# Kernel optimization log

Hardware: AMD Instinct MI355X
Metric: run time of the kernel (lower is better)

Reference implementation:

```python
import jax, jax.numpy as jnp
import numpy as np

B, N, C, H = 8, 1024, 768, 12
D = C // H
SCALE = D ** -0.5


def _norm_unbiased(t):
    # per-head-dim standardization with torch's default unbiased std (ddof=1)
    mu = t.mean(axis=-1, keepdims=True)
    var = ((t - mu) ** 2).sum(axis=-1, keepdims=True) / (t.shape[-1] - 1)
    return (t - mu) / jnp.sqrt(var)


def setup_inputs() -> dict:
    key = jax.random.key(0)
    kx, kq, kp, kb = jax.random.split(key, 4)
    x = jax.random.normal(kx, (B, N, C), dtype=jnp.float32)
    # nn.Linear default init ~ U(-1/sqrt(fan_in), 1/sqrt(fan_in)); scale suffices
    s = 1.0 / np.sqrt(C)
    qkv_w = jax.random.uniform(kq, (3 * C, C), minval=-s, maxval=s, dtype=jnp.float32)
    proj_w = jax.random.uniform(kp, (C, C), minval=-s, maxval=s, dtype=jnp.float32)
    proj_b = jax.random.uniform(kb, (C,), minval=-s, maxval=s, dtype=jnp.float32)
    return {"x": x, "qkv_w": qkv_w, "proj_w": proj_w, "proj_b": proj_b}


def reference(x, qkv_w, proj_w, proj_b):
    Bn, Nn, Cn = x.shape
    qkv = x @ qkv_w.T                                   # [B,N,3C]
    qkv = qkv.reshape(Bn, Nn, 3, H, D).transpose(2, 0, 3, 1, 4)  # [3,B,H,N,D]
    q, k, v = qkv[0], qkv[1], qkv[2]
    q = _norm_unbiased(q)
    k = _norm_unbiased(k)
    attn = jax.nn.softmax(jnp.einsum('bhnd,bhmd->bhnm', q, k) * SCALE, axis=-1)
    out = jnp.einsum('bhnm,bhmd->bhnd', attn, v)        # [B,H,N,D]
    out = out.transpose(0, 2, 1, 3).reshape(Bn, Nn, Cn)  # [B,N,C]
    return out @ proj_w.T + proj_b
```

## Files before the change

kernel.cpp:

```cpp
#include <hip/hip_runtime.h>
#include <hip/hip_bf16.h>
#include <stdint.h>

typedef unsigned short u16;
typedef __attribute__((ext_vector_type(8))) short bf16x8;
typedef __attribute__((ext_vector_type(4))) float f32x4;

#define GLDS16(gsrc, ldst) \
  __builtin_amdgcn_global_load_lds((const __attribute__((address_space(1))) uint32_t*)(gsrc), \
                                   (__attribute__((address_space(3))) uint32_t*)(ldst), 16, 0, 0)

__device__ __forceinline__ u16 f2bf(float f) {
  unsigned u = __float_as_uint(f);
  unsigned r = (u + 0x7fffu + ((u >> 16) & 1u)) >> 16;
  return (u16)r;
}
__device__ __forceinline__ float bf2f(u16 v) {
  return __uint_as_float(((unsigned)v) << 16);
}

__global__ void cvt_f2b4(const float* __restrict__ in, u16* __restrict__ out, int n4) {
  int i = blockIdx.x * 256 + threadIdx.x;
  if (i < n4) {
    float4 v = ((const float4*)in)[i];
    ushort4 r;
    r.x = f2bf(v.x); r.y = f2bf(v.y); r.z = f2bf(v.z); r.w = f2bf(v.w);
    ((ushort4*)out)[i] = r;
  }
}

template<int OUT_BF16, int HAS_BIAS>
__global__ __launch_bounds__(256, 2)
void gemm_bt(const u16* __restrict__ A, const u16* __restrict__ Bm,
             const float* __restrict__ bias, void* __restrict__ Cout,
             int M, int N, int K)
{
  __shared__ __align__(16) u16 As[128 * 32];
  __shared__ __align__(16) u16 Bs[128 * 32];
  const int tid  = threadIdx.x;
  const int lane = tid & 63;
  const int w    = tid >> 6;
  const int wr   = w >> 1, wc = w & 1;
  const int m0 = blockIdx.x * 128;
  const int n0 = blockIdx.y * 128;

  f32x4 acc[4][4];
  for (int m = 0; m < 4; ++m)
    for (int n = 0; n < 4; ++n)
      acc[m][n] = (f32x4){0.f, 0.f, 0.f, 0.f};

  const int rsel = lane >> 2;
  const int koff = (lane & 3) * 8;
  const int fr   = lane & 15;
  const int fk   = (lane >> 4) * 8;

  const int KT = K >> 5;
  for (int kt = 0; kt < KT; ++kt) {
    const int kbase = kt * 32;
#pragma unroll
    for (int t = 0; t < 2; ++t) {
      const int seg = w * 2 + t;
      const int rr = seg * 16 + rsel;
      GLDS16(A  + (size_t)(m0 + rr) * K + kbase + koff, (char*)As + seg * 1024);
      GLDS16(Bm + (size_t)(n0 + rr) * K + kbase + koff, (char*)Bs + seg * 1024);
    }
    __syncthreads();
    bf16x8 af[4], bg[4];
#pragma unroll
    for (int m = 0; m < 4; ++m)
      af[m] = *(const bf16x8*)(As + (wr * 64 + m * 16 + fr) * 32 + fk);
#pragma unroll
    for (int n = 0; n < 4; ++n)
      bg[n] = *(const bf16x8*)(Bs + (wc * 64 + n * 16 + fr) * 32 + fk);
#pragma unroll
    for (int m = 0; m < 4; ++m)
#pragma unroll
      for (int n = 0; n < 4; ++n)
        acc[m][n] = __builtin_amdgcn_mfma_f32_16x16x32_bf16(af[m], bg[n], acc[m][n], 0, 0, 0);
    __syncthreads();
  }

  const int r0 = m0 + wr * 64 + (lane >> 4) * 4;
  const int c0 = n0 + wc * 64 + fr;
  float bv[4];
  if (HAS_BIAS) {
#pragma unroll
    for (int n = 0; n < 4; ++n) bv[n] = bias[c0 + n * 16];
  }
#pragma unroll
  for (int m = 0; m < 4; ++m)
#pragma unroll
    for (int n = 0; n < 4; ++n)
#pragma unroll
      for (int i = 0; i < 4; ++i) {
        const size_t idx = (size_t)(r0 + m * 16 + i) * N + (c0 + n * 16);
        if (OUT_BF16) ((u16*)Cout)[idx] = f2bf(acc[m][n][i]);
        else          ((float*)Cout)[idx] = acc[m][n][i] + (HAS_BIAS ? bv[n] : 0.f);
      }
}

__global__ void norm_qk(const u16* __restrict__ qkv, u16* __restrict__ q, u16* __restrict__ k) {
  const int lane = threadIdx.x & 63;
  const int w = threadIdx.x >> 6;
  const int r = blockIdx.x * 4 + w;
  const int b = r / 12288;
  const int rem = r - b * 12288;
  const int h = rem >> 10;
  const int n = rem & 1023;
  const size_t rowbase = (size_t)(b * 1024 + n) * 2304 + h * 64 + lane;
  const size_t obase = ((size_t)(b * 12 + h) * 1024 + n) * 64 + lane;
#pragma unroll
  for (int s = 0; s < 2; ++s) {
    float t = bf2f(qkv[rowbase + (size_t)s * 768]);
    float sum = t;
#pragma unroll
    for (int m = 1; m < 64; m <<= 1) sum += __shfl_xor(sum, m, 64);
    float mu = sum * (1.f / 64.f);
    float d = t - mu;
    float ss = d * d;
#pragma unroll
    for (int m = 1; m < 64; m <<= 1) ss += __shfl_xor(ss, m, 64);
    float outv = d * rsqrtf(ss * (1.f / 63.f));
    (s == 0 ? q : k)[obase] = f2bf(outv);
  }
}

__global__ void transpose_v(const u16* __restrict__ qkv, u16* __restrict__ vt) {
  __shared__ u16 tile[64][65];
  const int bid = blockIdx.x;
  const int nt = bid & 15;
  const int bh = bid >> 4;
  const int b = bh / 12, h = bh % 12;
  const int tx = threadIdx.x & 63;
  const int ty = threadIdx.x >> 6;
#pragma unroll
  for (int i = 0; i < 16; ++i) {
    const int n = i * 4 + ty;
    tile[n][tx] = qkv[(size_t)(b * 1024 + nt * 64 + n) * 2304 + 1536 + h * 64 + tx];
  }
  __syncthreads();
#pragma unroll
  for (int i = 0; i < 16; ++i) {
    const int d = i * 4 + ty;
    vt[((size_t)(bh * 64 + d)) * 1024 + nt * 64 + tx] = tile[tx][d];
  }
}

__global__ __launch_bounds__(256, 2)
void attn_fwd(const u16* __restrict__ q, const u16* __restrict__ k,
              const u16* __restrict__ vt, u16* __restrict__ out)
{
  __shared__ __align__(16) u16 Ks[2][64 * 64];
  __shared__ __align__(16) u16 VTs[2][64 * 64];
  __shared__ __align__(16) u16 Ps[4][16 * 64];
  const int tid = threadIdx.x, lane = tid & 63, w = tid >> 6;
  const int bid = (blockIdx.x & 7) * 192 + (blockIdx.x >> 3);
  const int qt = bid & 15;
  const int bh = bid >> 4;
  const int b = bh / 12, h = bh % 12;
  const int fr = lane & 15;
  const int hi = lane >> 4;
  const int fk = hi * 8;

  bf16x8 aq[2];
  {
    const int qrow = qt * 64 + w * 16 + fr;
    const u16* qp = q + ((size_t)bh * 1024 + qrow) * 64;
#pragma unroll
    for (int kk = 0; kk < 2; ++kk)
      aq[kk] = *(const bf16x8*)(qp + kk * 32 + fk);
  }

  f32x4 o[4];
  for (int n = 0; n < 4; ++n) o[n] = (f32x4){0.f, 0.f, 0.f, 0.f};
  float rs[4] = {0.f, 0.f, 0.f, 0.f};

  const int srow = lane >> 3;
  const int sc   = ((lane & 7) ^ srow) * 8;
  const u16* kg = k  + (size_t)bh * 65536;
  const u16* vg = vt + (size_t)bh * 65536;

  auto stage = [&](int buf, int kt) {
#pragma unroll
    for (int t = 0; t < 2; ++t) {
      const int seg = w * 2 + t;
      const int rr = seg * 8 + srow;
      GLDS16(kg + (size_t)(kt * 64 + rr) * 64 + sc,  (char*)Ks[buf]  + seg * 1024);
      GLDS16(vg + (size_t)rr * 1024 + kt * 64 + sc,  (char*)VTs[buf] + seg * 1024);
    }
  };

  int cur = 0;
  stage(0, 0);
  for (int kt = 0; kt < 16; ++kt) {
    __syncthreads();
    if (kt < 15) stage(cur ^ 1, kt + 1);

    f32x4 s[4];
#pragma unroll
    for (int n = 0; n < 4; ++n) s[n] = (f32x4){0.f, 0.f, 0.f, 0.f};
#pragma unroll
    for (int n = 0; n < 4; ++n)
#pragma unroll
      for (int kk = 0; kk < 2; ++kk) {
        bf16x8 bk = *(const bf16x8*)(Ks[cur] + (n * 16 + fr) * 64 + (((kk * 4 + hi) ^ (fr & 7)) * 8));
        s[n] = __builtin_amdgcn_mfma_f32_16x16x32_bf16(aq[kk], bk, s[n], 0, 0, 0);
      }

#pragma unroll
    for (int n = 0; n < 4; ++n)
#pragma unroll
      for (int i = 0; i < 4; ++i) {
        float p = __expf(s[n][i] * 0.125f);
        rs[i] += p;
        const int row = hi * 4 + i;
        const int swc = (n * 2 + (fr >> 3)) ^ (row & 7);
        Ps[w][row * 64 + swc * 8 + (fr & 7)] = f2bf(p);
      }

#pragma unroll
    for (int kk = 0; kk < 2; ++kk) {
      bf16x8 ap = *(const bf16x8*)(&Ps[w][fr * 64 + (((kk * 4 + hi) ^ (fr & 7)) * 8)]);
#pragma unroll
      for (int n = 0; n < 4; ++n) {
        bf16x8 bv = *(const bf16x8*)(VTs[cur] + (n * 16 + fr) * 64 + (((kk * 4 + hi) ^ (fr & 7)) * 8));
        o[n] = __builtin_amdgcn_mfma_f32_16x16x32_bf16(ap, bv, o[n], 0, 0, 0);
      }
    }
    cur ^= 1;
  }

  float inv[4];
#pragma unroll
  for (int i = 0; i < 4; ++i) {
    float v = rs[i];
    v += __shfl_xor(v, 1, 64);
    v += __shfl_xor(v, 2, 64);
    v += __shfl_xor(v, 4, 64);
    v += __shfl_xor(v, 8, 64);
    inv[i] = 1.f / v;
  }
  const int orow0 = qt * 64 + w * 16 + (lane >> 4) * 4;
#pragma unroll
  for (int n = 0; n < 4; ++n)
#pragma unroll
    for (int i = 0; i < 4; ++i)
      out[((size_t)b * 1024 + orow0 + i) * 768 + h * 64 + n * 16 + fr] = f2bf(o[n][i] * inv[i]);
}

extern "C" void kernel_launch(void* const* d_in, const int* in_sizes, int n_in,
                              void* d_out, int out_size, void* d_ws, size_t ws_size,
                              hipStream_t stream)
{
  (void)in_sizes; (void)n_in; (void)out_size; (void)ws_size;
  const float* x      = (const float*)d_in[0];
  const float* qkv_w  = (const float*)d_in[1];
  const float* proj_w = (const float*)d_in[2];
  const float* proj_b = (const float*)d_in[3];
  float* out = (float*)d_out;

  char* p = (char*)d_ws;
  auto take = [&](size_t bytes) { char* r = p; p += (bytes + 255) & ~(size_t)255; return r; };
  u16* xb   = (u16*)take((size_t)8192 * 768 * 2);
  u16* wqb  = (u16*)take((size_t)2304 * 768 * 2);
  u16* wpb  = (u16*)take((size_t)768 * 768 * 2);
  u16* qkvb = (u16*)take((size_t)8192 * 2304 * 2);
  u16* qb   = (u16*)take((size_t)8192 * 768 * 2);
  u16* kb   = (u16*)take((size_t)8192 * 768 * 2);
  u16* vtb  = (u16*)take((size_t)8192 * 768 * 2);
  u16* aob  = (u16*)take((size_t)8192 * 768 * 2);

  cvt_f2b4<<<6144, 256, 0, stream>>>(x, xb, 8192 * 768 / 4);
  cvt_f2b4<<<1728, 256, 0, stream>>>(qkv_w, wqb, 2304 * 768 / 4);
  cvt_f2b4<<<576,  256, 0, stream>>>(proj_w, wpb, 768 * 768 / 4);

  gemm_bt<1, 0><<<dim3(64, 18), 256, 0, stream>>>(xb, wqb, nullptr, qkvb, 8192, 2304, 768);
  norm_qk<<<24576, 256, 0, stream>>>(qkvb, qb, kb);
  transpose_v<<<1536, 256, 0, stream>>>(qkvb, vtb);
  attn_fwd<<<1536, 256, 0, stream>>>(qb, kb, vtb, aob);
  gemm_bt<0, 1><<<dim3(64, 6), 256, 0, stream>>>(aob, wpb, proj_b, out, 8192, 768, 768);
}
```

Measured before the change: 233.4 us.

## Fuse V transpose and head layout into QKV GEMM epilogue, triple-buffer GEMM loads

The QKV GEMM now writes q and k in per-head layout and V already transposed, so the separate transpose kernel and the strided reads in normalization go away. Both GEMMs get a three-stage global-to-LDS pipeline with manual vmcnt waits, and their occupancy hint rises to 3. The normalization kernel is vectorized to four elements per lane, with 16 lanes per row. In attention, the softmax row sums are computed by an extra MFMA against a ones vector instead of scalar adds plus shuffles, and bf16 rounding is simplified to round-half-up. The simpler rounding and summing the bf16-rounded probabilities slightly change numerics.

```diff
diff --git a/kernel.cpp b/kernel.cpp
--- a/kernel.cpp
+++ b/kernel.cpp
@@ -12,8 +12,10 @@
 
 __device__ __forceinline__ u16 f2bf(float f) {
   unsigned u = __float_as_uint(f);
-  unsigned r = (u + 0x7fffu + ((u >> 16) & 1u)) >> 16;
-  return (u16)r;
+  return (u16)((u + 0x7fffu + ((u >> 16) & 1u)) >> 16);
+}
+__device__ __forceinline__ u16 f2bfr(float f) {
+  return (u16)((__float_as_uint(f) + 0x8000u) >> 16);
 }
 __device__ __forceinline__ float bf2f(u16 v) {
   return __uint_as_float(((unsigned)v) << 16);
@@ -29,120 +31,138 @@
   }
 }
 
-template<int OUT_BF16, int HAS_BIAS>
-__global__ __launch_bounds__(256, 2)
-void gemm_bt(const u16* __restrict__ A, const u16* __restrict__ Bm,
-             const float* __restrict__ bias, void* __restrict__ Cout,
-             int M, int N, int K)
-{
-  __shared__ __align__(16) u16 As[128 * 32];
-  __shared__ __align__(16) u16 Bs[128 * 32];
-  const int tid  = threadIdx.x;
-  const int lane = tid & 63;
-  const int w    = tid >> 6;
-  const int wr   = w >> 1, wc = w & 1;
-  const int m0 = blockIdx.x * 128;
-  const int n0 = blockIdx.y * 128;
-
-  f32x4 acc[4][4];
-  for (int m = 0; m < 4; ++m)
-    for (int n = 0; n < 4; ++n)
-      acc[m][n] = (f32x4){0.f, 0.f, 0.f, 0.f};
-
-  const int rsel = lane >> 2;
-  const int koff = (lane & 3) * 8;
-  const int fr   = lane & 15;
-  const int fk   = (lane >> 4) * 8;
-
-  const int KT = K >> 5;
-  for (int kt = 0; kt < KT; ++kt) {
-    const int kbase = kt * 32;
-#pragma unroll
-    for (int t = 0; t < 2; ++t) {
-      const int seg = w * 2 + t;
-      const int rr = seg * 16 + rsel;
-      GLDS16(A  + (size_t)(m0 + rr) * K + kbase + koff, (char*)As + seg * 1024);
-      GLDS16(Bm + (size_t)(n0 + rr) * K + kbase + koff, (char*)Bs + seg * 1024);
+
+#define GEMM_PREAMBLE(AP, BP)                                              \
+  __shared__ __align__(16) u16 As[3][128 * 32];                            \
+  __shared__ __align__(16) u16 Bs[3][128 * 32];                            \
+  const int tid  = threadIdx.x;                                            \
+  const int lane = tid & 63;                                               \
+  const int w    = tid >> 6;                                               \
+  const int wr   = w >> 1, wc = w & 1;                                     \
+  const int m0 = blockIdx.x * 128;                                         \
+  const int n0 = blockIdx.y * 128;                                         \
+  f32x4 acc[4][4];                                                         \
+  for (int m = 0; m < 4; ++m)                                              \
+    for (int n = 0; n < 4; ++n) acc[m][n] = (f32x4){0.f, 0.f, 0.f, 0.f};   \
+  const int rsel = lane >> 2;                                              \
+  const int koff = (lane & 3) * 8;                                         \
+  const int fr   = lane & 15;                                              \
+  const int hi   = lane >> 4;                                              \
+  const int fk   = hi * 8;                                                 \
+  auto stage = [&](int buf, int kt) {                                      \
+    _Pragma("unroll")                                                      \
+    for (int t = 0; t < 2; ++t) {                                          \
+      const int seg = w * 2 + t;                                           \
+      const int rr  = seg * 16 + rsel;                                     \
+      GLDS16(AP + (size_t)(m0 + rr) * 768 + kt * 32 + koff,                \
+             (char*)As[buf] + seg * 1024);                                 \
+      GLDS16(BP + (size_t)(n0 + rr) * 768 + kt * 32 + koff,                \
+             (char*)Bs[buf] + seg * 1024);                                 \
+    }                                                                      \
+  };                                                                       \
+  stage(0, 0); stage(1, 1);                                                \
+  asm volatile("s_waitcnt vmcnt(4)" ::: "memory");                         \
+  __builtin_amdgcn_s_barrier();                                            \
+  for (int kt = 0; kt < 24; ++kt) {                                        \
+    const int cb = kt % 3;                                                 \
+    if (kt + 2 < 24) stage((kt + 2) % 3, kt + 2);                          \
+    bf16x8 af[4], bg[4];                                                   \
+    _Pragma("unroll")                                                      \
+    for (int m = 0; m < 4; ++m)                                            \
+      af[m] = *(const bf16x8*)(As[cb] + (wr * 64 + m * 16 + fr) * 32 + fk);\
+    _Pragma("unroll")                                                      \
+    for (int n = 0; n < 4; ++n)                                            \
+      bg[n] = *(const bf16x8*)(Bs[cb] + (wc * 64 + n * 16 + fr) * 32 + fk);\
+    _Pragma("unroll")                                                      \
+    for (int m = 0; m < 4; ++m)                                            \
+      _Pragma("unroll")                                                    \
+      for (int n = 0; n < 4; ++n)                                          \
+        acc[m][n] = __builtin_amdgcn_mfma_f32_16x16x32_bf16(af[m], bg[n], acc[m][n], 0, 0, 0); \
+    if (kt < 23) {                                                         \
+      if (kt < 22) asm volatile("s_waitcnt vmcnt(4)" ::: "memory");        \
+      else         asm volatile("s_waitcnt vmcnt(0)" ::: "memory");        \
+      __builtin_amdgcn_s_barrier();                                        \
+    }                                                                      \
+  }
+
+__global__ __launch_bounds__(256, 3)
+void gemm_qkv(const u16* __restrict__ A, const u16* __restrict__ Bm,
+              u16* __restrict__ qraw, u16* __restrict__ kraw, u16* __restrict__ vt)
+{
+  GEMM_PREAMBLE(A, Bm)
+  const int b     = m0 >> 10;
+  const int nrow0 = (m0 & 1023) + wr * 64 + hi * 4;
+  const int sec   = n0 / 768;
+  const int csb   = (n0 % 768) + wc * 64;
+  u16* const secp = (sec == 0) ? qraw : (sec == 1) ? kraw : vt;
+#pragma unroll
+  for (int nf = 0; nf < 4; ++nf) {
+    const int cs = csb + nf * 16;
+    const int h  = cs >> 6;
+    const int d  = (cs & 63) + fr;
+    u16* base = secp + ((size_t)(b * 12 + h) << 16);
+    if (sec < 2) {
+#pragma unroll
+      for (int m = 0; m < 4; ++m)
+#pragma unroll
+        for (int i = 0; i < 4; ++i)
+          base[(size_t)(nrow0 + m * 16 + i) * 64 + d] = f2bfr(acc[m][nf][i]);
+    } else {
+#pragma unroll
+      for (int m = 0; m < 4; ++m) {
+        ushort4 pk;
+        pk.x = f2bfr(acc[m][nf][0]); pk.y = f2bfr(acc[m][nf][1]);
+        pk.z = f2bfr(acc[m][nf][2]); pk.w = f2bfr(acc[m][nf][3]);
+        *(ushort4*)(base + (size_t)d * 1024 + nrow0 + m * 16) = pk;
+      }
     }
-    __syncthreads();
-    bf16x8 af[4], bg[4];
+  }
+}
+
+__global__ __launch_bounds__(256, 3)
+void gemm_proj(const u16* __restrict__ A, const u16* __restrict__ Bm,
+               const float* __restrict__ bias, float* __restrict__ Cout)
+{
+  GEMM_PREAMBLE(A, Bm)
+  const int r0 = m0 + wr * 64 + hi * 4;
+  const int c0 = n0 + wc * 64 + fr;
+#pragma unroll
+  for (int nf = 0; nf < 4; ++nf) {
+    const float bv = bias[c0 + nf * 16];
 #pragma unroll
     for (int m = 0; m < 4; ++m)
-      af[m] = *(const bf16x8*)(As + (wr * 64 + m * 16 + fr) * 32 + fk);
-#pragma unroll
-    for (int n = 0; n < 4; ++n)
-      bg[n] = *(const bf16x8*)(Bs + (wc * 64 + n * 16 + fr) * 32 + fk);
-#pragma unroll
-    for (int m = 0; m < 4; ++m)
-#pragma unroll
-      for (int n = 0; n < 4; ++n)
-        acc[m][n] = __builtin_amdgcn_mfma_f32_16x16x32_bf16(af[m], bg[n], acc[m][n], 0, 0, 0);
-    __syncthreads();
-  }
-
-  const int r0 = m0 + wr * 64 + (lane >> 4) * 4;
-  const int c0 = n0 + wc * 64 + fr;
-  float bv[4];
-  if (HAS_BIAS) {
-#pragma unroll
-    for (int n = 0; n < 4; ++n) bv[n] = bias[c0 + n * 16];
-  }
-#pragma unroll
-  for (int m = 0; m < 4; ++m)
-#pragma unroll
-    for (int n = 0; n < 4; ++n)
-#pragma unroll
-      for (int i = 0; i < 4; ++i) {
-        const size_t idx = (size_t)(r0 + m * 16 + i) * N + (c0 + n * 16);
-        if (OUT_BF16) ((u16*)Cout)[idx] = f2bf(acc[m][n][i]);
-        else          ((float*)Cout)[idx] = acc[m][n][i] + (HAS_BIAS ? bv[n] : 0.f);
-      }
-}
-
-__global__ void norm_qk(const u16* __restrict__ qkv, u16* __restrict__ q, u16* __restrict__ k) {
-  const int lane = threadIdx.x & 63;
-  const int w = threadIdx.x >> 6;
-  const int r = blockIdx.x * 4 + w;
-  const int b = r / 12288;
-  const int rem = r - b * 12288;
-  const int h = rem >> 10;
-  const int n = rem & 1023;
-  const size_t rowbase = (size_t)(b * 1024 + n) * 2304 + h * 64 + lane;
-  const size_t obase = ((size_t)(b * 12 + h) * 1024 + n) * 64 + lane;
+#pragma unroll
+      for (int i = 0; i < 4; ++i)
+        Cout[(size_t)(r0 + m * 16 + i) * 768 + c0 + nf * 16] = acc[m][nf][i] + bv;
+  }
+}
+
+__global__ void norm_qk(const u16* __restrict__ qraw, const u16* __restrict__ kraw,
+                        u16* __restrict__ q, u16* __restrict__ k)
+{
+  const int lane = threadIdx.x & 63, w = threadIdx.x >> 6;
+  const int g = lane >> 4, sub = lane & 15;
+  const int r = blockIdx.x * 16 + w * 4 + g;
+  const size_t base = (size_t)r * 64 + sub * 4;
 #pragma unroll
   for (int s = 0; s < 2; ++s) {
-    float t = bf2f(qkv[rowbase + (size_t)s * 768]);
-    float sum = t;
-#pragma unroll
-    for (int m = 1; m < 64; m <<= 1) sum += __shfl_xor(sum, m, 64);
-    float mu = sum * (1.f / 64.f);
-    float d = t - mu;
-    float ss = d * d;
-#pragma unroll
-    for (int m = 1; m < 64; m <<= 1) ss += __shfl_xor(ss, m, 64);
-    float outv = d * rsqrtf(ss * (1.f / 63.f));
-    (s == 0 ? q : k)[obase] = f2bf(outv);
-  }
-}
-
-__global__ void transpose_v(const u16* __restrict__ qkv, u16* __restrict__ vt) {
-  __shared__ u16 tile[64][65];
-  const int bid = blockIdx.x;
-  const int nt = bid & 15;
-  const int bh = bid >> 4;
-  const int b = bh / 12, h = bh % 12;
-  const int tx = threadIdx.x & 63;
-  const int ty = threadIdx.x >> 6;
-#pragma unroll
-  for (int i = 0; i < 16; ++i) {
-    const int n = i * 4 + ty;
-    tile[n][tx] = qkv[(size_t)(b * 1024 + nt * 64 + n) * 2304 + 1536 + h * 64 + tx];
-  }
-  __syncthreads();
-#pragma unroll
-  for (int i = 0; i < 16; ++i) {
-    const int d = i * 4 + ty;
-    vt[((size_t)(bh * 64 + d)) * 1024 + nt * 64 + tx] = tile[tx][d];
+    const u16* src = s ? kraw : qraw;
+    u16* dst = s ? k : q;
+    ushort4 v = *(const ushort4*)(src + base);
+    float f0 = bf2f(v.x), f1 = bf2f(v.y), f2 = bf2f(v.z), f3 = bf2f(v.w);
+    float sum = f0 + f1 + f2 + f3;
+    sum += __shfl_xor(sum, 1, 64); sum += __shfl_xor(sum, 2, 64);
+    sum += __shfl_xor(sum, 4, 64); sum += __shfl_xor(sum, 8, 64);
+    const float mu = sum * (1.f / 64.f);
+    f0 -= mu; f1 -= mu; f2 -= mu; f3 -= mu;
+    float ss = f0 * f0 + f1 * f1 + f2 * f2 + f3 * f3;
+    ss += __shfl_xor(ss, 1, 64); ss += __shfl_xor(ss, 2, 64);
+    ss += __shfl_xor(ss, 4, 64); ss += __shfl_xor(ss, 8, 64);
+    const float sc = rsqrtf(ss * (1.f / 63.f));
+    ushort4 o;
+    o.x = f2bfr(f0 * sc); o.y = f2bfr(f1 * sc);
+    o.z = f2bfr(f2 * sc); o.w = f2bfr(f3 * sc);
+    *(ushort4*)(dst + base) = o;
   }
 }
 
@@ -171,9 +191,13 @@
       aq[kk] = *(const bf16x8*)(qp + kk * 32 + fk);
   }
 
+  bf16x8 ones;
+#pragma unroll
+  for (int j = 0; j < 8; ++j) ones[j] = (short)0x3F80;
+
   f32x4 o[4];
   for (int n = 0; n < 4; ++n) o[n] = (f32x4){0.f, 0.f, 0.f, 0.f};
-  float rs[4] = {0.f, 0.f, 0.f, 0.f};
+  f32x4 o5 = (f32x4){0.f, 0.f, 0.f, 0.f};
 
   const int srow = lane >> 3;
   const int sc   = ((lane & 7) ^ srow) * 8;
@@ -211,16 +235,16 @@
     for (int n = 0; n < 4; ++n)
 #pragma unroll
       for (int i = 0; i < 4; ++i) {
-        float p = __expf(s[n][i] * 0.125f);
-        rs[i] += p;
+        const float p = __expf(s[n][i] * 0.125f);
         const int row = hi * 4 + i;
         const int swc = (n * 2 + (fr >> 3)) ^ (row & 7);
-        Ps[w][row * 64 + swc * 8 + (fr & 7)] = f2bf(p);
+        Ps[w][row * 64 + swc * 8 + (fr & 7)] = f2bfr(p);
       }
 
 #pragma unroll
     for (int kk = 0; kk < 2; ++kk) {
       bf16x8 ap = *(const bf16x8*)(&Ps[w][fr * 64 + (((kk * 4 + hi) ^ (fr & 7)) * 8)]);
+      o5 = __builtin_amdgcn_mfma_f32_16x16x32_bf16(ap, ones, o5, 0, 0, 0);
 #pragma unroll
       for (int n = 0; n < 4; ++n) {
         bf16x8 bv = *(const bf16x8*)(VTs[cur] + (n * 16 + fr) * 64 + (((kk * 4 + hi) ^ (fr & 7)) * 8));
@@ -232,20 +256,13 @@
 
   float inv[4];
 #pragma unroll
-  for (int i = 0; i < 4; ++i) {
-    float v = rs[i];
-    v += __shfl_xor(v, 1, 64);
-    v += __shfl_xor(v, 2, 64);
-    v += __shfl_xor(v, 4, 64);
-    v += __shfl_xor(v, 8, 64);
-    inv[i] = 1.f / v;
-  }
-  const int orow0 = qt * 64 + w * 16 + (lane >> 4) * 4;
+  for (int i = 0; i < 4; ++i) inv[i] = 1.f / o5[i];
+  const int orow0 = qt * 64 + w * 16 + hi * 4;
 #pragma unroll
   for (int n = 0; n < 4; ++n)
 #pragma unroll
     for (int i = 0; i < 4; ++i)
-      out[((size_t)b * 1024 + orow0 + i) * 768 + h * 64 + n * 16 + fr] = f2bf(o[n][i] * inv[i]);
+      out[((size_t)b * 1024 + orow0 + i) * 768 + h * 64 + n * 16 + fr] = f2bfr(o[n][i] * inv[i]);
 }
 
 extern "C" void kernel_launch(void* const* d_in, const int* in_sizes, int n_in,
@@ -264,19 +281,19 @@
   u16* xb   = (u16*)take((size_t)8192 * 768 * 2);
   u16* wqb  = (u16*)take((size_t)2304 * 768 * 2);
   u16* wpb  = (u16*)take((size_t)768 * 768 * 2);
-  u16* qkvb = (u16*)take((size_t)8192 * 2304 * 2);
+  u16* qraw = (u16*)take((size_t)8192 * 768 * 2);
+  u16* kraw = (u16*)take((size_t)8192 * 768 * 2);
+  u16* vtb  = (u16*)take((size_t)8192 * 768 * 2);
   u16* qb   = (u16*)take((size_t)8192 * 768 * 2);
   u16* kb   = (u16*)take((size_t)8192 * 768 * 2);
-  u16* vtb  = (u16*)take((size_t)8192 * 768 * 2);
   u16* aob  = (u16*)take((size_t)8192 * 768 * 2);
 
   cvt_f2b4<<<6144, 256, 0, stream>>>(x, xb, 8192 * 768 / 4);
   cvt_f2b4<<<1728, 256, 0, stream>>>(qkv_w, wqb, 2304 * 768 / 4);
   cvt_f2b4<<<576,  256, 0, stream>>>(proj_w, wpb, 768 * 768 / 4);
 
-  gemm_bt<1, 0><<<dim3(64, 18), 256, 0, stream>>>(xb, wqb, nullptr, qkvb, 8192, 2304, 768);
-  norm_qk<<<24576, 256, 0, stream>>>(qkvb, qb, kb);
-  transpose_v<<<1536, 256, 0, stream>>>(qkvb, vtb);
+  gemm_qkv<<<dim3(64, 18), 256, 0, stream>>>(xb, wqb, qraw, kraw, vtb);
+  norm_qk<<<6144, 256, 0, stream>>>(qraw, kraw, qb, kb);
   attn_fwd<<<1536, 256, 0, stream>>>(qb, kb, vtb, aob);
-  gemm_bt<0, 1><<<dim3(64, 6), 256, 0, stream>>>(aob, wpb, proj_b, out, 8192, 768, 768);
-}
+  gemm_proj<<<dim3(64, 6), 256, 0, stream>>>(aob, wpb, proj_b, out);
+}
```

Result: faster. 204.7 us (-12.3%).
